# Performance work log

Hardware: AMD Instinct MI355X
Metric: run time of the kernel (lower is better)

The kernel has to match this reference:

```python
import jax, jax.numpy as jnp
import numpy as np

N, CIN, COUT, K, CSTYLE, H, W = 8, 512, 512, 3, 512, 64, 64
EPS = 1e-8
SQRT2 = 2.0 ** 0.5


def setup_inputs() -> dict:
    key = jax.random.key(0)
    ks = jax.random.split(key, 5)
    return {
        "x": jax.random.normal(ks[0], (N, CIN, H, W), jnp.float32),
        "style": jax.random.normal(ks[1], (N, CSTYLE), jnp.float32),
        "noise": jax.random.normal(ks[2], (N, 1, H, W), jnp.float32),
        "conv_weight": jax.random.normal(ks[3], (1, COUT, CIN, K, K), jnp.float32),
        "mod_weight": jax.random.normal(ks[4], (CIN, CSTYLE), jnp.float32) / np.float32(np.sqrt(CSTYLE)),
        "mod_bias": jnp.ones((CIN,), jnp.float32),
        "noise_weight": jnp.zeros((1,), jnp.float32),
        "act_bias": jnp.zeros((COUT,), jnp.float32),
    }


def reference(x, style, noise, conv_weight, mod_weight, mod_bias, noise_weight, act_bias):
    n = x.shape[0]
    # style modulation: linear(style) -> per-sample per-in-channel scale (style_bias=0)
    s = style @ mod_weight.T + mod_bias                       # (n, cin)
    # modulate shared weight (1, cout, cin, k, k) -> (n, cout, cin, k, k)
    w = conv_weight * s[:, None, :, None, None]
    # demodulate
    demod = jax.lax.rsqrt(jnp.sum(w * w, axis=(2, 3, 4)) + EPS)  # (n, cout)
    w = w * demod[:, :, None, None, None]
    # grouped conv: groups = batch
    w = w.reshape(n * COUT, CIN, K, K)
    xg = x.reshape(1, n * CIN, H, W)
    out = jax.lax.conv_general_dilated(
        xg, w,
        window_strides=(1, 1),
        padding=[(K // 2, K // 2), (K // 2, K // 2)],
        dimension_numbers=("NCHW", "OIHW", "NCHW"),
        feature_group_count=n,
    )
    out = out.reshape(n, COUT, H, W) * SQRT2
    # noise injection (scalar weight, broadcast noise)
    out = out + noise_weight[0] * noise
    # fused bias + leaky relu (slope 0.2)
    out = jax.nn.leaky_relu(out + act_bias[None, :, None, None], negative_slope=0.2)
    return out
```

## Files before the change

### kernel.cpp

```cpp
#include <hip/hip_runtime.h>
#include <hip/hip_bf16.h>
#include <stdint.h>


typedef __attribute__((ext_vector_type(8))) short short8;
typedef __attribute__((ext_vector_type(4))) float f32x4;
typedef __attribute__((ext_vector_type(4))) unsigned int uint4v;
typedef __attribute__((ext_vector_type(2))) unsigned int uint2v;

__device__ __forceinline__ unsigned short f2bf(float f) {
  unsigned u = __builtin_bit_cast(unsigned, f);
  u += 0x7FFFu + ((u >> 16) & 1u);
  return (unsigned short)(u >> 16);
}

__device__ __forceinline__ void g2l16(const void* g, void* l) {
  __builtin_amdgcn_global_load_lds(
      (const __attribute__((address_space(1))) void*)g,
      (__attribute__((address_space(3))) void*)l, 16, 0, 0);
}

__global__ void k_pre(const float* __restrict__ style, const float* __restrict__ mw,
                      const float* __restrict__ mb, const float* __restrict__ cw,
                      float* __restrict__ s_out, float* __restrict__ wsq) {
  int t = threadIdx.x;
  int b = blockIdx.x;
  if (b < 1024) {
    int wid = b * 4 + (t >> 6);
    int lane = t & 63;
    int n = wid >> 9, ci = wid & 511;
    float sum = 0.f;
#pragma unroll
    for (int i = 0; i < 8; ++i) {
      int k = lane + i * 64;
      sum += style[n * 512 + k] * mw[ci * 512 + k];
    }
#pragma unroll
    for (int off = 32; off; off >>= 1) sum += __shfl_xor(sum, off, 64);
    if (lane == 0) s_out[wid] = sum + mb[ci];
  } else {
    int id = (b - 1024) * 256 + t;
    const float* p = cw + (size_t)id * 9;
    float a = 0.f;
#pragma unroll
    for (int j = 0; j < 9; ++j) a += p[j] * p[j];
    wsq[id] = a;
  }
}

__global__ void k_mid(const float* __restrict__ s, const float* __restrict__ wsq,
                      const float* __restrict__ x, const float* __restrict__ cw,
                      float* __restrict__ demod, unsigned short* __restrict__ Xp,
                      unsigned short* __restrict__ Wt) {
  __shared__ char smem[74240];
  int t = threadIdx.x;
  int b = blockIdx.x;
  if (b < 512) {
    int n = b >> 6, h = b & 63;
    short* ldsx = (short*)smem;
    float* sxf = (float*)(smem + 69632);
    sxf[t] = s[n * 512 + t];
    sxf[t + 256] = s[n * 512 + 256 + t];
    __syncthreads();
    const float* xb = x + ((size_t)n * 512) * 4096 + h * 64;
#pragma unroll
    for (int i = 0; i < 32; ++i) {
      int L = t + i * 256;
      int ci = L >> 4, q = L & 15;
      f32x4 v = *(const f32x4*)(xb + (size_t)ci * 4096 + q * 4);
      float sv = sxf[ci];
      uint2v o;
      o.x = f2bf(v.x * sv) | ((unsigned)f2bf(v.y * sv) << 16);
      o.y = f2bf(v.z * sv) | ((unsigned)f2bf(v.w * sv) << 16);
      *(uint2v*)(ldsx + ci * 68 + q * 4) = o;
    }
    __syncthreads();
    unsigned short* nb = Xp + (size_t)n * 2230272 + (size_t)(h + 1) * 33792;
#pragma unroll
    for (int r = 0; r < 16; ++r) {
      int u = t + r * 256;
      int cig = u >> 6, col = u & 63;
      unsigned v[8];
#pragma unroll
      for (int j = 0; j < 8; ++j)
        v[j] = (unsigned short)ldsx[(cig * 8 + j) * 68 + col];
      uint4v o;
      o.x = v[0] | (v[1] << 16);
      o.y = v[2] | (v[3] << 16);
      o.z = v[4] | (v[5] << 16);
      o.w = v[6] | (v[7] << 16);
      *(uint4v*)(nb + ((size_t)cig * 66 + col + 1) * 8) = o;
    }
  } else if (b < 1536) {
    int wid = (b - 512) * 4 + (t >> 6);
    int lane = t & 63;
    int n = wid >> 9, co = wid & 511;
    float sum = 0.f;
#pragma unroll
    for (int i = 0; i < 8; ++i) {
      int ci = lane + i * 64;
      float sv = s[n * 512 + ci];
      sum += sv * sv * wsq[co * 512 + ci];
    }
#pragma unroll
    for (int off = 32; off; off >>= 1) sum += __shfl_xor(sum, off, 64);
    if (lane == 0) demod[wid] = rsqrtf(sum + 1e-8f) * 1.41421356237309515f;
  } else if (b < 1664) {
    int bb = b - 1536;
    int cb = bb >> 4, kb = bb & 15;
    float* ldsf = (float*)smem;
#pragma unroll
    for (int i = 0; i < 72; ++i) {
      int idx = t + i * 256;
      int seg = idx / 288, off = idx - seg * 288;
      ldsf[seg * 289 + off] = cw[(size_t)(cb * 64 + seg) * 4608 + kb * 288 + off];
    }
    __syncthreads();
    unsigned short* ob = Wt + (size_t)(cb * 16 + kb) * 18432;
#pragma unroll
    for (int i = 0; i < 9; ++i) {
      int c = t + i * 256;
      int m = c & 15, lhi = (c >> 4) & 3, mt = (c >> 6) & 3, tap = c >> 8;
      int co_rel = mt * 16 + m;
      unsigned v[8];
#pragma unroll
      for (int j = 0; j < 8; ++j)
        v[j] = f2bf(ldsf[co_rel * 289 + (lhi * 8 + j) * 9 + tap]);
      uint4v o;
      o.x = v[0] | (v[1] << 16);
      o.y = v[2] | (v[3] << 16);
      o.z = v[4] | (v[5] << 16);
      o.w = v[6] | (v[7] << 16);
      *(uint4v*)(ob + (size_t)c * 8) = o;
    }
  } else {
    int bb = b - 1664;
    int n = bb / 17, part = bb % 17;
    uint4v z = (uint4v){0u, 0u, 0u, 0u};
    unsigned short* base = Xp + (size_t)n * 2230272;
#pragma unroll
    for (int i = 0; i < 4; ++i) {
      int id = part * 1024 + i * 256 + t;
      if (id < 16640) {
        size_t off;
        if (id < 8448) {
          int row = (id < 4224) ? 0 : 65;
          int c = id - ((id < 4224) ? 0 : 4224);
          off = (size_t)row * 33792 + (size_t)c * 8;
        } else {
          int id2 = id - 8448;
          int row = 1 + (id2 >> 7);
          int rem = id2 & 127;
          int klhi = rem >> 1;
          int col = (rem & 1) ? 65 : 0;
          off = (size_t)row * 33792 + ((size_t)klhi * 66 + col) * 8;
        }
        *(uint4v*)(base + off) = z;
      }
    }
  }
}

__global__ void __launch_bounds__(256, 2) k_conv(
    const unsigned short* __restrict__ Wt, const unsigned short* __restrict__ Xp,
    const float* __restrict__ demod, const float* __restrict__ noise,
    const float* __restrict__ nw_p, const float* __restrict__ act_bias,
    float* __restrict__ out) {
  __shared__ short lds_a[18432];
  __shared__ short lds_x[22528];
  int t = threadIdx.x;
  int r0 = blockIdx.x * 8;
  int cb = blockIdx.y;
  int n = blockIdx.z;
  int lane = t & 63, wv = t >> 6;
  int l15 = lane & 15, lhi = lane >> 4;

  const unsigned short* abase = Wt + (size_t)cb * 16 * 18432;
  const unsigned short* xbase = Xp + (size_t)n * 2230272;
  int xoffg[11];
#pragma unroll
  for (int j = 0; j < 11; ++j) {
    int c = j * 256 + t;
    int r = c / 264, rc = c - r * 264;
    int off = (r0 + r) * 33792 + rc * 8;
    if (c >= 2640) off = 0;
    xoffg[j] = off;
  }

  f32x4 acc[4][8];
#pragma unroll
  for (int a = 0; a < 4; ++a)
#pragma unroll
    for (int bq = 0; bq < 8; ++bq) acc[a][bq] = (f32x4){0.f, 0.f, 0.f, 0.f};

  const int aoff = lhi * 128 + l15 * 8;
  const int xoffb = lhi * 528 + (wv * 16 + l15) * 8;

  for (int kb = 0; kb < 16; ++kb) {
    __syncthreads();
    const char* ab = (const char*)(abase + (size_t)kb * 18432);
#pragma unroll
    for (int i = 0; i < 9; ++i)
      g2l16(ab + i * 4096 + t * 16, (char*)lds_a + i * 4096 + t * 16);
#pragma unroll
    for (int j = 0; j < 11; ++j)
      g2l16(xbase + xoffg[j] + kb * 2112, (char*)lds_x + j * 4096 + t * 16);
    __syncthreads();

#pragma unroll
    for (int dw = 0; dw < 3; ++dw) {
      short8 bf[10];
#pragma unroll
      for (int rr = 0; rr < 10; ++rr)
        bf[rr] = *(const short8*)(lds_x + rr * 2112 + dw * 8 + xoffb);
#pragma unroll
      for (int dh = 0; dh < 3; ++dh) {
#pragma unroll
        for (int mt = 0; mt < 4; ++mt) {
          short8 af = *(const short8*)(lds_a + (dh * 3 + dw) * 2048 + mt * 512 + aoff);
#pragma unroll
          for (int ri = 0; ri < 8; ++ri)
            acc[mt][ri] =
                __builtin_amdgcn_mfma_f32_16x16x32_bf16(af, bf[ri + dh], acc[mt][ri], 0, 0, 0);
        }
      }
    }
  }

  float nw = nw_p[0];
  int col = wv * 16 + l15;
  float nz[8];
#pragma unroll
  for (int ri = 0; ri < 8; ++ri)
    nz[ri] = nw * noise[((size_t)n * 64 + r0 + ri) * 64 + col];
#pragma unroll
  for (int mt = 0; mt < 4; ++mt) {
    f32x4 dm4 = *(const f32x4*)(demod + n * 512 + cb * 64 + mt * 16 + lhi * 4);
#pragma unroll
    for (int c = 0; c < 4; ++c) {
      int co = cb * 64 + mt * 16 + lhi * 4 + c;
      float ab2 = act_bias[co];
      float dm = dm4[c];
#pragma unroll
      for (int ri = 0; ri < 8; ++ri) {
        float v = dm * acc[mt][ri][c] + nz[ri] + ab2;
        v = v > 0.f ? v : 0.2f * v;
        out[(((size_t)n * 512 + co) * 64 + (r0 + ri)) * 64 + col] = v;
      }
    }
  }
}

extern "C" void kernel_launch(void* const* d_in, const int* in_sizes, int n_in,
                              void* d_out, int out_size, void* d_ws, size_t ws_size,
                              hipStream_t stream) {
  const float* x     = (const float*)d_in[0];
  const float* style = (const float*)d_in[1];
  const float* noise = (const float*)d_in[2];
  const float* cw    = (const float*)d_in[3];
  const float* mw    = (const float*)d_in[4];
  const float* mb    = (const float*)d_in[5];
  const float* nw    = (const float*)d_in[6];
  const float* ab    = (const float*)d_in[7];
  float* out = (float*)d_out;

  char* ws = (char*)d_ws;
  float* s_buf  = (float*)ws;
  float* demod  = (float*)(ws + 16384);
  float* wsq    = (float*)(ws + 32768);
  unsigned short* Wt = (unsigned short*)(ws + 1081344);
  unsigned short* Xp = (unsigned short*)(ws + 5799936);

  k_pre<<<2048, 256, 0, stream>>>(style, mw, mb, cw, s_buf, wsq);
  k_mid<<<1800, 256, 0, stream>>>(s_buf, wsq, x, cw, demod, Xp, Wt);
  k_conv<<<dim3(8, 8, 8), 256, 0, stream>>>(Wt, Xp, demod, noise, nw, ab, out);
}
```

Baseline: 267.9 us.

## Fuse style modulation and demodulation into the input-packing prep kernel

Merges the two preprocessing kernels into one: each x-packing block now recomputes the per-sample style vector s from style and mod_weight, then computes demod for 8 output channels from the squared conv weights on the fly. This removes one kernel launch and the wsq/s intermediate buffers, and cuts the grid from 1800 to 776 blocks. In exchange, every block redundantly computes the full 512x512 style matvec and per-channel weight squared sums, which adds compute and global reads to each of the 512 packing blocks.

```diff
diff --git a/kernel.cpp b/kernel.cpp
--- a/kernel.cpp
+++ b/kernel.cpp
@@ -20,48 +20,56 @@
       (__attribute__((address_space(3))) void*)l, 16, 0, 0);
 }
 
-__global__ void k_pre(const float* __restrict__ style, const float* __restrict__ mw,
-                      const float* __restrict__ mb, const float* __restrict__ cw,
-                      float* __restrict__ s_out, float* __restrict__ wsq) {
-  int t = threadIdx.x;
-  int b = blockIdx.x;
-  if (b < 1024) {
-    int wid = b * 4 + (t >> 6);
-    int lane = t & 63;
-    int n = wid >> 9, ci = wid & 511;
-    float sum = 0.f;
-#pragma unroll
-    for (int i = 0; i < 8; ++i) {
-      int k = lane + i * 64;
-      sum += style[n * 512 + k] * mw[ci * 512 + k];
-    }
-#pragma unroll
-    for (int off = 32; off; off >>= 1) sum += __shfl_xor(sum, off, 64);
-    if (lane == 0) s_out[wid] = sum + mb[ci];
-  } else {
-    int id = (b - 1024) * 256 + t;
-    const float* p = cw + (size_t)id * 9;
-    float a = 0.f;
-#pragma unroll
-    for (int j = 0; j < 9; ++j) a += p[j] * p[j];
-    wsq[id] = a;
-  }
-}
-
-__global__ void k_mid(const float* __restrict__ s, const float* __restrict__ wsq,
-                      const float* __restrict__ x, const float* __restrict__ cw,
-                      float* __restrict__ demod, unsigned short* __restrict__ Xp,
-                      unsigned short* __restrict__ Wt) {
-  __shared__ char smem[74240];
+__global__ void k_prep(const float* __restrict__ style, const float* __restrict__ mw,
+                       const float* __restrict__ mb, const float* __restrict__ cw,
+                       const float* __restrict__ x, float* __restrict__ demod_g,
+                       unsigned short* __restrict__ Xp, unsigned short* __restrict__ Wt) {
+  __shared__ __align__(16) char smem[74240];
   int t = threadIdx.x;
   int b = blockIdx.x;
   if (b < 512) {
     int n = b >> 6, h = b & 63;
     short* ldsx = (short*)smem;
-    float* sxf = (float*)(smem + 69632);
-    sxf[t] = s[n * 512 + t];
-    sxf[t + 256] = s[n * 512 + 256 + t];
-    __syncthreads();
+    float* sxf  = (float*)(smem + 69632);
+    float* stl  = (float*)(smem + 71680);
+    stl[t] = style[n * 512 + t];
+    stl[t + 256] = style[n * 512 + 256 + t];
+    __syncthreads();
+#pragma unroll
+    for (int rr = 0; rr < 2; ++rr) {
+      int ci = t + rr * 256;
+      const float* mr = mw + (size_t)ci * 512;
+      float a0 = 0.f, a1 = 0.f, a2 = 0.f, a3 = 0.f;
+#pragma unroll 8
+      for (int k2 = 0; k2 < 128; ++k2) {
+        f32x4 wv = *(const f32x4*)(mr + k2 * 4);
+        f32x4 sv = *(const f32x4*)(stl + k2 * 4);
+        a0 += wv.x * sv.x; a1 += wv.y * sv.y;
+        a2 += wv.z * sv.z; a3 += wv.w * sv.w;
+      }
+      sxf[ci] = (a0 + a1) + (a2 + a3) + mb[ci];
+    }
+    __syncthreads();
+    {
+      int g = t >> 5, l5 = t & 31;
+      int co = h * 8 + g;
+      const float* cwb = cw + (size_t)co * 4608;
+      float sum = 0.f;
+#pragma unroll
+      for (int i = 0; i < 16; ++i) {
+        int ci = l5 + i * 32;
+        const float* p = cwb + ci * 9;
+        float a = 0.f;
+#pragma unroll
+        for (int j = 0; j < 9; ++j) a += p[j] * p[j];
+        float sv = sxf[ci];
+        sum += sv * sv * a;
+      }
+#pragma unroll
+      for (int off = 16; off; off >>= 1) sum += __shfl_xor(sum, off, 64);
+      if (l5 == 0)
+        demod_g[n * 512 + co] = rsqrtf(sum + 1e-8f) * 1.41421356237309515f;
+    }
     const float* xb = x + ((size_t)n * 512) * 4096 + h * 64;
 #pragma unroll
     for (int i = 0; i < 32; ++i) {
@@ -91,22 +99,8 @@
       o.w = v[6] | (v[7] << 16);
       *(uint4v*)(nb + ((size_t)cig * 66 + col + 1) * 8) = o;
     }
-  } else if (b < 1536) {
-    int wid = (b - 512) * 4 + (t >> 6);
-    int lane = t & 63;
-    int n = wid >> 9, co = wid & 511;
-    float sum = 0.f;
-#pragma unroll
-    for (int i = 0; i < 8; ++i) {
-      int ci = lane + i * 64;
-      float sv = s[n * 512 + ci];
-      sum += sv * sv * wsq[co * 512 + ci];
-    }
-#pragma unroll
-    for (int off = 32; off; off >>= 1) sum += __shfl_xor(sum, off, 64);
-    if (lane == 0) demod[wid] = rsqrtf(sum + 1e-8f) * 1.41421356237309515f;
-  } else if (b < 1664) {
-    int bb = b - 1536;
+  } else if (b < 640) {
+    int bb = b - 512;
     int cb = bb >> 4, kb = bb & 15;
     float* ldsf = (float*)smem;
 #pragma unroll
@@ -134,7 +128,7 @@
       *(uint4v*)(ob + (size_t)c * 8) = o;
     }
   } else {
-    int bb = b - 1664;
+    int bb = b - 640;
     int n = bb / 17, part = bb % 17;
     uint4v z = (uint4v){0u, 0u, 0u, 0u};
     unsigned short* base = Xp + (size_t)n * 2230272;
@@ -265,13 +259,10 @@
   float* out = (float*)d_out;
 
   char* ws = (char*)d_ws;
-  float* s_buf  = (float*)ws;
   float* demod  = (float*)(ws + 16384);
-  float* wsq    = (float*)(ws + 32768);
   unsigned short* Wt = (unsigned short*)(ws + 1081344);
   unsigned short* Xp = (unsigned short*)(ws + 5799936);
 
-  k_pre<<<2048, 256, 0, stream>>>(style, mw, mb, cw, s_buf, wsq);
-  k_mid<<<1800, 256, 0, stream>>>(s_buf, wsq, x, cw, demod, Xp, Wt);
+  k_prep<<<776, 256, 0, stream>>>(style, mw, mb, cw, x, demod, Xp, Wt);
   k_conv<<<dim3(8, 8, 8), 256, 0, stream>>>(Wt, Xp, demod, noise, nw, ab, out);
 }
```

Result: slower. 309.3 us (+15.5%).
